# Kernel optimization log

Measured on AMD Instinct MI355X. Metric: run time of the kernel, lower is better.

The kernel has to match this reference:

```python
import jax, jax.numpy as jnp
import numpy as np

N_NODES = 100000
N_EDGES = 1600000
IN_CH = 64
HID = 64
N_CLASSES = 10
N_GRAPHS = 64


def setup_inputs() -> dict:
    key = jax.random.key(0)
    ks = jax.random.split(key, 12)
    x = jax.random.normal(ks[0], (N_NODES, IN_CH), dtype=jnp.float32)
    edge_index = jax.random.randint(ks[1], (2, N_EDGES), 0, N_NODES, dtype=jnp.int64)
    batch = jnp.sort(jax.random.randint(ks[2], (N_NODES,), 0, N_GRAPHS, dtype=jnp.int64))
    def glorot(k, shape):
        lim = 1.0 / np.sqrt(shape[1])
        return jax.random.uniform(k, shape, dtype=jnp.float32, minval=-lim, maxval=lim)
    # GraphConv layer 1: lin_rel (with bias) and lin_root (no bias)
    W1_rel = glorot(ks[3], (HID, IN_CH))
    W1_root = glorot(ks[4], (HID, IN_CH))
    b1 = glorot(ks[5], (1, IN_CH))[0, :HID] * 0 + glorot(ks[5], (HID, 1))[:, 0]
    # GraphConv layer 2
    W2_rel = glorot(ks[6], (HID, HID))
    W2_root = glorot(ks[7], (HID, HID))
    b2 = glorot(ks[8], (HID, 1))[:, 0]
    # final classifier Linear
    W_lin = glorot(ks[9], (N_CLASSES, HID))
    b_lin = glorot(ks[10], (N_CLASSES, 1))[:, 0]
    return {
        "x": x, "edge_index": edge_index, "batch": batch,
        "W1_rel": W1_rel, "W1_root": W1_root, "b1": b1,
        "W2_rel": W2_rel, "W2_root": W2_root, "b2": b2,
        "W_lin": W_lin, "b_lin": b_lin,
    }


def _graph_conv(x, src, dst, W_rel, W_root, b):
    # PyG GraphConv: out_i = W_rel @ (sum_{j->i} x_j) + b + W_root @ x_i
    agg = jax.ops.segment_sum(x[src], dst, num_segments=N_NODES)  # [N, C]
    return agg @ W_rel.T + x @ W_root.T + b


def reference(x, edge_index, batch, W1_rel, W1_root, b1, W2_rel, W2_root, b2, W_lin, b_lin):
    src, dst = edge_index[0], edge_index[1]
    h = jax.nn.relu(_graph_conv(x, src, dst, W1_rel, W1_root, b1))
    h = jax.nn.relu(_graph_conv(h, src, dst, W2_rel, W2_root, b2))
    # global mean pool over graph ids
    sums = jax.ops.segment_sum(h, batch, num_segments=N_GRAPHS)          # [G, H]
    counts = jax.ops.segment_sum(jnp.ones((h.shape[0],), h.dtype), batch, num_segments=N_GRAPHS)
    pooled = sums / jnp.maximum(counts, 1.0)[:, None]
    return pooled @ W_lin.T + b_lin  # [G, num_classes]
```

## Files before the change

### kernel.cpp

```cpp
#include <hip/hip_runtime.h>

typedef unsigned short u16;
typedef __attribute__((ext_vector_type(8))) short bf16x8;
typedef __attribute__((ext_vector_type(4))) float f32x4;

constexpr int CH = 64;
constexpr int NG = 64;
constexpr int NC = 10;
constexpr int SHIFT = 9;
constexpr int BW = 1 << SHIFT;
constexpr int EPW = 8192;

__device__ __forceinline__ void f4add(float4& a, const float4 v) {
    a.x += v.x; a.y += v.y; a.z += v.z; a.w += v.w;
}
__device__ __forceinline__ u16 f2bf(float f) {
    unsigned u = __float_as_uint(f);
    u = (u + 0x7FFFu + ((u >> 16) & 1u)) >> 16;
    return (u16)u;
}
__device__ __forceinline__ void bfacc(float4& a, unsigned lo, unsigned hi) {
    a.x += __uint_as_float(lo << 16);
    a.y += __uint_as_float(lo & 0xFFFF0000u);
    a.z += __uint_as_float(hi << 16);
    a.w += __uint_as_float(hi & 0xFFFF0000u);
}

__global__ __launch_bounds__(256) void k_bucket(const int* __restrict__ src,
                                                const int* __restrict__ dst,
                                                int* __restrict__ bcnt,
                                                int* __restrict__ bbuf,
                                                int nb, int cap, int n_edges)
{
    __shared__ int hist[256];
    __shared__ int cur[256];
    int t = threadIdx.x;
    int e0 = blockIdx.x * EPW;
    int e1 = min(e0 + EPW, n_edges);
    if (t < nb) hist[t] = 0;
    __syncthreads();
    for (int e = e0 + t; e < e1; e += 256)
        atomicAdd(&hist[dst[e] >> SHIFT], 1);
    __syncthreads();
    if (t < nb) cur[t] = atomicAdd(&bcnt[t], hist[t]);
    __syncthreads();
    for (int e = e0 + t; e < e1; e += 256) {
        int d = dst[e];
        int b = d >> SHIFT;
        int pos = atomicAdd(&cur[b], 1);
        if (pos < cap)
            bbuf[(size_t)b * cap + pos] = src[e] | ((d & (BW - 1)) << 17);
    }
}

__global__ __launch_bounds__(256) void k_bscan(const int* __restrict__ bcnt,
                                               int* __restrict__ bbase,
                                               int* __restrict__ rowptr,
                                               int nb, int n, int cap)
{
    __shared__ int lds[256];
    int t = threadIdx.x;
    int v = (t < nb) ? min(bcnt[t], cap) : 0;
    lds[t] = v;
    __syncthreads();
    for (int off = 1; off < 256; off <<= 1) {
        int u = (t >= off) ? lds[t - off] : 0;
        __syncthreads();
        lds[t] += u;
        __syncthreads();
    }
    if (t < nb) bbase[t] = lds[t] - v;
    if (t == nb - 1) { bbase[nb] = lds[t]; rowptr[n] = lds[t]; }
}

__global__ __launch_bounds__(256) void k_build(const int* __restrict__ bbuf,
                                               const int* __restrict__ bcnt,
                                               const int* __restrict__ bbase,
                                               int* __restrict__ rowptr,
                                               int* __restrict__ csr,
                                               int cap, int n)
{
    __shared__ int hist[BW];
    __shared__ int cur[BW];
    __shared__ int psum[256];
    int b = blockIdx.x;
    int t = threadIdx.x;
    int cnt = min(bcnt[b], cap);
    int base = bbase[b];
    const int* mybuf = bbuf + (size_t)b * cap;
    hist[t] = 0; hist[t + 256] = 0;
    __syncthreads();
    for (int i = t; i < cnt; i += 256)
        atomicAdd(&hist[mybuf[i] >> 17], 1);
    __syncthreads();
    int h0 = hist[2 * t], h1 = hist[2 * t + 1];
    int ps = h0 + h1;
    psum[t] = ps;
    __syncthreads();
    for (int off = 1; off < 256; off <<= 1) {
        int u = (t >= off) ? psum[t - off] : 0;
        __syncthreads();
        psum[t] += u;
        __syncthreads();
    }
    int e0 = psum[t] - ps;
    int nodeBase = b * BW;
    cur[2 * t]     = base + e0;
    cur[2 * t + 1] = base + e0 + h0;
    if (nodeBase + 2 * t < n)     rowptr[nodeBase + 2 * t]     = base + e0;
    if (nodeBase + 2 * t + 1 < n) rowptr[nodeBase + 2 * t + 1] = base + e0 + h0;
    __syncthreads();
    for (int i = t; i < cnt; i += 256) {
        int v = mybuf[i];
        int pos = atomicAdd(&cur[v >> 17], 1);
        csr[pos] = v & 0x1FFFF;
    }
}

template<bool BF16IN>
__global__ __launch_bounds__(256) void k_xform_mfma(const void* in_,
                                                    const float* __restrict__ Wrel,
                                                    const float* __restrict__ Wroot,
                                                    const float* __restrict__ bias,
                                                    u16* __restrict__ Y,
                                                    u16* R, int n, int ngroups)
{
    int lane = threadIdx.x & 63;
    int lr = lane & 15;
    int g  = lane >> 4;

    bf16x8 wf[2][4][2];
    const float* Wm[2] = { Wrel, Wroot };
#pragma unroll
    for (int m = 0; m < 2; ++m)
#pragma unroll
        for (int t = 0; t < 4; ++t)
#pragma unroll
            for (int kt = 0; kt < 2; ++kt) {
                const float* p = Wm[m] + (16 * t + lr) * CH + 32 * kt + 8 * g;
                bf16x8 v;
#pragma unroll
                for (int j = 0; j < 8; ++j) v[j] = (short)f2bf(p[j]);
                wf[m][t][kt] = v;
            }
    float bvt[4];
#pragma unroll
    for (int t = 0; t < 4; ++t) bvt[t] = bias[16 * t + lr];

    int wid = blockIdx.x * 4 + (threadIdx.x >> 6);
#pragma unroll
    for (int gi = 0; gi < 2; ++gi) {
        int grp = wid * 2 + gi;
        if (grp >= ngroups) return;
        int gbase = grp * 16;
        int arow = gbase + lr;
        if (arow >= n) arow = n - 1;

        bf16x8 af[2];
#pragma unroll
        for (int kt = 0; kt < 2; ++kt) {
            if (BF16IN) {
                const u16* hp = (const u16*)in_ + (size_t)arow * CH + kt * 32 + 8 * g;
                af[kt] = *(const bf16x8*)hp;
            } else {
                const float* xp = (const float*)in_ + (size_t)arow * CH + kt * 32 + 8 * g;
                bf16x8 v;
#pragma unroll
                for (int j = 0; j < 8; ++j) v[j] = (short)f2bf(xp[j]);
                af[kt] = v;
            }
        }

        f32x4 z = { 0.f, 0.f, 0.f, 0.f };
        f32x4 aY[4] = { z, z, z, z };
        f32x4 aR[4] = { z, z, z, z };
#pragma unroll
        for (int kt = 0; kt < 2; ++kt)
#pragma unroll
            for (int t = 0; t < 4; ++t) {
                aY[t] = __builtin_amdgcn_mfma_f32_16x16x32_bf16(af[kt], wf[0][t][kt], aY[t], 0, 0, 0);
                aR[t] = __builtin_amdgcn_mfma_f32_16x16x32_bf16(af[kt], wf[1][t][kt], aR[t], 0, 0, 0);
            }

#pragma unroll
        for (int t = 0; t < 4; ++t)
#pragma unroll
            for (int r = 0; r < 4; ++r) {
                int node = gbase + 4 * g + r;
                if (node < n) {
                    Y[(size_t)node * CH + 16 * t + lr] = f2bf(aY[t][r]);
                    R[(size_t)node * CH + 16 * t + lr] = f2bf(aR[t][r] + bvt[t]);
                }
            }
    }
}

__global__ __launch_bounds__(256) void k_gather_relu(const u16* __restrict__ Y,
                                                     const int* __restrict__ rowptr,
                                                     const int* __restrict__ csr,
                                                     u16* __restrict__ RO, int n)
{
    int lane = threadIdx.x & 63;
    int grp = lane >> 4, sub = lane & 15;
    int wid = blockIdx.x * 4 + (threadIdx.x >> 6);
    int nw = gridDim.x * 4;
    for (int node = wid; node < n; node += nw) {
        int e0 = rowptr[node], e1 = rowptr[node + 1];
        float4 a0 = make_float4(0, 0, 0, 0), a1 = a0, a2 = a0, a3 = a0;
        int e = e0;
        for (; e + 16 <= e1; e += 16) {
            int s0 = csr[e + grp],      s1 = csr[e + 4 + grp];
            int s2 = csr[e + 8 + grp],  s3 = csr[e + 12 + grp];
            uint2 p0 = *(const uint2*)(Y + (size_t)s0 * CH + sub * 4);
            uint2 p1 = *(const uint2*)(Y + (size_t)s1 * CH + sub * 4);
            uint2 p2 = *(const uint2*)(Y + (size_t)s2 * CH + sub * 4);
            uint2 p3 = *(const uint2*)(Y + (size_t)s3 * CH + sub * 4);
            bfacc(a0, p0.x, p0.y); bfacc(a1, p1.x, p1.y);
            bfacc(a2, p2.x, p2.y); bfacc(a3, p3.x, p3.y);
        }
        for (; e + 4 <= e1; e += 4) {
            int s = csr[e + grp];
            uint2 p = *(const uint2*)(Y + (size_t)s * CH + sub * 4);
            bfacc(a0, p.x, p.y);
        }
        if (e + grp < e1) {
            int s = csr[e + grp];
            uint2 p = *(const uint2*)(Y + (size_t)s * CH + sub * 4);
            bfacc(a1, p.x, p.y);
        }
        f4add(a0, a1); f4add(a2, a3); f4add(a0, a2);
        a0.x += __shfl_xor(a0.x, 16); a0.y += __shfl_xor(a0.y, 16);
        a0.z += __shfl_xor(a0.z, 16); a0.w += __shfl_xor(a0.w, 16);
        a0.x += __shfl_xor(a0.x, 32); a0.y += __shfl_xor(a0.y, 32);
        a0.z += __shfl_xor(a0.z, 32); a0.w += __shfl_xor(a0.w, 32);
        if (grp == 0) {
            uint2 pr = *(const uint2*)(RO + (size_t)node * CH + sub * 4);
            float4 r = make_float4(0, 0, 0, 0);
            bfacc(r, pr.x, pr.y);
            float4 h;
            h.x = fmaxf(a0.x + r.x, 0.f); h.y = fmaxf(a0.y + r.y, 0.f);
            h.z = fmaxf(a0.z + r.z, 0.f); h.w = fmaxf(a0.w + r.w, 0.f);
            uint2 o;
            o.x = (unsigned)f2bf(h.x) | ((unsigned)f2bf(h.y) << 16);
            o.y = (unsigned)f2bf(h.z) | ((unsigned)f2bf(h.w) << 16);
            *(uint2*)(RO + (size_t)node * CH + sub * 4) = o;
        }
    }
}

__global__ __launch_bounds__(256) void k_gather_pool(const u16* __restrict__ Y,
                                                     const u16* __restrict__ R,
                                                     const int* __restrict__ rowptr,
                                                     const int* __restrict__ csr,
                                                     const int* __restrict__ batch,
                                                     float* __restrict__ sums,
                                                     int n, int chunk)
{
    int lane = threadIdx.x & 63;
    int grp = lane >> 4, sub = lane & 15;
    int wid = blockIdx.x * 4 + (threadIdx.x >> 6);
    int nb = wid * chunk, ne = min(nb + chunk, n);
    float4 run = make_float4(0, 0, 0, 0);
    int gcur = -1;
    for (int node = nb; node < ne; ++node) {
        int e0 = rowptr[node], e1 = rowptr[node + 1];
        float4 a0 = make_float4(0, 0, 0, 0), a1 = a0, a2 = a0, a3 = a0;
        int e = e0;
        for (; e + 16 <= e1; e += 16) {
            int s0 = csr[e + grp],      s1 = csr[e + 4 + grp];
            int s2 = csr[e + 8 + grp],  s3 = csr[e + 12 + grp];
            uint2 p0 = *(const uint2*)(Y + (size_t)s0 * CH + sub * 4);
            uint2 p1 = *(const uint2*)(Y + (size_t)s1 * CH + sub * 4);
            uint2 p2 = *(const uint2*)(Y + (size_t)s2 * CH + sub * 4);
            uint2 p3 = *(const uint2*)(Y + (size_t)s3 * CH + sub * 4);
            bfacc(a0, p0.x, p0.y); bfacc(a1, p1.x, p1.y);
            bfacc(a2, p2.x, p2.y); bfacc(a3, p3.x, p3.y);
        }
        for (; e + 4 <= e1; e += 4) {
            int s = csr[e + grp];
            uint2 p = *(const uint2*)(Y + (size_t)s * CH + sub * 4);
            bfacc(a0, p.x, p.y);
        }
        if (e + grp < e1) {
            int s = csr[e + grp];
            uint2 p = *(const uint2*)(Y + (size_t)s * CH + sub * 4);
            bfacc(a1, p.x, p.y);
        }
        f4add(a0, a1); f4add(a2, a3); f4add(a0, a2);
        a0.x += __shfl_xor(a0.x, 16); a0.y += __shfl_xor(a0.y, 16);
        a0.z += __shfl_xor(a0.z, 16); a0.w += __shfl_xor(a0.w, 16);
        a0.x += __shfl_xor(a0.x, 32); a0.y += __shfl_xor(a0.y, 32);
        a0.z += __shfl_xor(a0.z, 32); a0.w += __shfl_xor(a0.w, 32);
        if (grp == 0) {
            uint2 pr = *(const uint2*)(R + (size_t)node * CH + sub * 4);
            float4 r = make_float4(0, 0, 0, 0);
            bfacc(r, pr.x, pr.y);
            float4 h;
            h.x = fmaxf(a0.x + r.x, 0.f); h.y = fmaxf(a0.y + r.y, 0.f);
            h.z = fmaxf(a0.z + r.z, 0.f); h.w = fmaxf(a0.w + r.w, 0.f);
            int g = batch[node];
            if (g != gcur) {
                if (gcur >= 0) {
                    atomicAdd(&sums[gcur * CH + sub * 4 + 0], run.x);
                    atomicAdd(&sums[gcur * CH + sub * 4 + 1], run.y);
                    atomicAdd(&sums[gcur * CH + sub * 4 + 2], run.z);
                    atomicAdd(&sums[gcur * CH + sub * 4 + 3], run.w);
                }
                run = make_float4(0, 0, 0, 0);
                gcur = g;
            }
            f4add(run, h);
        }
    }
    if (grp == 0 && gcur >= 0) {
        atomicAdd(&sums[gcur * CH + sub * 4 + 0], run.x);
        atomicAdd(&sums[gcur * CH + sub * 4 + 1], run.y);
        atomicAdd(&sums[gcur * CH + sub * 4 + 2], run.z);
        atomicAdd(&sums[gcur * CH + sub * 4 + 3], run.w);
    }
}

__global__ void k_final(const float* __restrict__ sums,
                        const int* __restrict__ batch,
                        const float* __restrict__ Wlin,
                        const float* __restrict__ blin,
                        float* __restrict__ out, int n_nodes)
{
    int t = threadIdx.x;
    if (t >= NG * NC) return;
    int g = t / NC, c = t % NC;
    int lo = 0, hi = n_nodes;
    while (lo < hi) { int mid = (lo + hi) >> 1; if (batch[mid] < g) lo = mid + 1; else hi = mid; }
    int lb = lo;
    lo = 0; hi = n_nodes;
    while (lo < hi) { int mid = (lo + hi) >> 1; if (batch[mid] < g + 1) lo = mid + 1; else hi = mid; }
    int cnt = lo - lb;
    float inv = 1.0f / fmaxf((float)cnt, 1.0f);
    float acc = blin[c];
    for (int k = 0; k < CH; ++k)
        acc += sums[g * CH + k] * inv * Wlin[c * CH + k];
    out[g * NC + c] = acc;
}

extern "C" void kernel_launch(void* const* d_in, const int* in_sizes, int n_in,
                              void* d_out, int out_size, void* d_ws, size_t ws_size,
                              hipStream_t stream)
{
    const float* x      = (const float*)d_in[0];
    const int*   ei     = (const int*)d_in[1];
    const int*   batch  = (const int*)d_in[2];
    const float* W1rel  = (const float*)d_in[3];
    const float* W1root = (const float*)d_in[4];
    const float* b1     = (const float*)d_in[5];
    const float* W2rel  = (const float*)d_in[6];
    const float* W2root = (const float*)d_in[7];
    const float* b2     = (const float*)d_in[8];
    const float* Wlin   = (const float*)d_in[9];
    const float* blin   = (const float*)d_in[10];
    float* out = (float*)d_out;

    int n_nodes = in_sizes[0] / CH;
    int n_edges = in_sizes[1] / 2;
    const int* src = ei;
    const int* dst = ei + n_edges;

    int nb  = (n_nodes + BW - 1) >> SHIFT;
    int cap = n_edges / nb + 2048;

    u16*   Ybf    = (u16*)d_ws;
    u16*   Rbf    = Ybf + (size_t)n_nodes * CH;
    int*   rowptr = (int*)(Rbf + (size_t)n_nodes * CH);
    int*   csr    = rowptr + (n_nodes + 1);
    int*   bbuf   = csr + n_edges;
    int*   bcnt   = bbuf + (size_t)nb * cap;
    int*   bbase  = bcnt + 256;
    float* sums   = (float*)(bbase + 257);

    hipMemsetAsync(bcnt, 0, 256 * sizeof(int), stream);
    int b1blocks = (n_edges + EPW - 1) / EPW;
    k_bucket<<<b1blocks, 256, 0, stream>>>(src, dst, bcnt, bbuf, nb, cap, n_edges);
    k_bscan<<<1, 256, 0, stream>>>(bcnt, bbase, rowptr, nb, n_nodes, cap);
    k_build<<<nb, 256, 0, stream>>>(bbuf, bcnt, bbase, rowptr, csr, cap, n_nodes);

    int ngroups = (n_nodes + 15) / 16;
    int xblocks = (ngroups + 7) / 8;

    k_xform_mfma<false><<<xblocks, 256, 0, stream>>>(x, W1rel, W1root, b1,
                                                     Ybf, Rbf, n_nodes, ngroups);
    k_gather_relu<<<2048, 256, 0, stream>>>(Ybf, rowptr, csr, Rbf, n_nodes);

    k_xform_mfma<true><<<xblocks, 256, 0, stream>>>(Rbf, W2rel, W2root, b2,
                                                    Ybf, Rbf, n_nodes, ngroups);
    hipMemsetAsync(sums, 0, NG * CH * sizeof(float), stream);
    int waves = 2048 * 4;
    int chunk = (n_nodes + waves - 1) / waves;
    k_gather_pool<<<2048, 256, 0, stream>>>(Ybf, Rbf, rowptr, csr, batch, sums, n_nodes, chunk);

    k_final<<<1, NG * NC, 0, stream>>>(sums, batch, Wlin, blin, out, n_nodes);
}
```

Before: 237.3 us.

## Assign each 16-lane group its own node chunk in gather kernels

The gather kernels now have each 16-lane quarter-wave own a contiguous 4-node chunk and walk its edges serially, replacing the old scheme where all four groups split one node's edges and then reduced with cross-lane shuffles. This drops the shuffle reduction and the idle lanes during the epilogue, and it reuses rowptr between consecutive nodes. The two gather kernels are merged into one template with a POOL flag. The cost is more divergence between groups with different degrees, and a launch grid sized to the node count rather than a fixed 2048 blocks.

```diff
diff --git a/kernel.cpp b/kernel.cpp
--- a/kernel.cpp
+++ b/kernel.cpp
@@ -195,116 +195,64 @@
     }
 }
 
-__global__ __launch_bounds__(256) void k_gather_relu(const u16* __restrict__ Y,
-                                                     const int* __restrict__ rowptr,
-                                                     const int* __restrict__ csr,
-                                                     u16* __restrict__ RO, int n)
+template<bool POOL>
+__global__ __launch_bounds__(256) void k_gather2(const u16* __restrict__ Y,
+                                                 const int* __restrict__ rowptr,
+                                                 const int* __restrict__ csr,
+                                                 u16* RO,
+                                                 const int* __restrict__ batch,
+                                                 float* __restrict__ sums,
+                                                 int n, int chunk)
 {
     int lane = threadIdx.x & 63;
-    int grp = lane >> 4, sub = lane & 15;
-    int wid = blockIdx.x * 4 + (threadIdx.x >> 6);
-    int nw = gridDim.x * 4;
-    for (int node = wid; node < n; node += nw) {
-        int e0 = rowptr[node], e1 = rowptr[node + 1];
-        float4 a0 = make_float4(0, 0, 0, 0), a1 = a0, a2 = a0, a3 = a0;
+    int sub = lane & 15;
+    int grp = lane >> 4;
+    int gid = (blockIdx.x * 4 + (threadIdx.x >> 6)) * 4 + grp;
+    int nb = gid * chunk;
+    if (nb >= n) return;
+    int ne = min(nb + chunk, n);
+    float4 run = make_float4(0, 0, 0, 0);
+    int gcur = -1;
+    int e0 = rowptr[nb];
+    for (int node = nb; node < ne; ++node) {
+        int e1 = rowptr[node + 1];
+        float4 accA = make_float4(0, 0, 0, 0), accB = accA;
         int e = e0;
-        for (; e + 16 <= e1; e += 16) {
-            int s0 = csr[e + grp],      s1 = csr[e + 4 + grp];
-            int s2 = csr[e + 8 + grp],  s3 = csr[e + 12 + grp];
+        for (; e + 4 <= e1; e += 4) {
+            int s0 = csr[e + 0], s1 = csr[e + 1];
+            int s2 = csr[e + 2], s3 = csr[e + 3];
             uint2 p0 = *(const uint2*)(Y + (size_t)s0 * CH + sub * 4);
             uint2 p1 = *(const uint2*)(Y + (size_t)s1 * CH + sub * 4);
             uint2 p2 = *(const uint2*)(Y + (size_t)s2 * CH + sub * 4);
             uint2 p3 = *(const uint2*)(Y + (size_t)s3 * CH + sub * 4);
-            bfacc(a0, p0.x, p0.y); bfacc(a1, p1.x, p1.y);
-            bfacc(a2, p2.x, p2.y); bfacc(a3, p3.x, p3.y);
+            bfacc(accA, p0.x, p0.y); bfacc(accB, p1.x, p1.y);
+            bfacc(accA, p2.x, p2.y); bfacc(accB, p3.x, p3.y);
         }
-        for (; e + 4 <= e1; e += 4) {
-            int s = csr[e + grp];
+        for (; e < e1; ++e) {
+            int s = csr[e];
             uint2 p = *(const uint2*)(Y + (size_t)s * CH + sub * 4);
-            bfacc(a0, p.x, p.y);
+            bfacc(accA, p.x, p.y);
         }
-        if (e + grp < e1) {
-            int s = csr[e + grp];
-            uint2 p = *(const uint2*)(Y + (size_t)s * CH + sub * 4);
-            bfacc(a1, p.x, p.y);
-        }
-        f4add(a0, a1); f4add(a2, a3); f4add(a0, a2);
-        a0.x += __shfl_xor(a0.x, 16); a0.y += __shfl_xor(a0.y, 16);
-        a0.z += __shfl_xor(a0.z, 16); a0.w += __shfl_xor(a0.w, 16);
-        a0.x += __shfl_xor(a0.x, 32); a0.y += __shfl_xor(a0.y, 32);
-        a0.z += __shfl_xor(a0.z, 32); a0.w += __shfl_xor(a0.w, 32);
-        if (grp == 0) {
-            uint2 pr = *(const uint2*)(RO + (size_t)node * CH + sub * 4);
-            float4 r = make_float4(0, 0, 0, 0);
-            bfacc(r, pr.x, pr.y);
-            float4 h;
-            h.x = fmaxf(a0.x + r.x, 0.f); h.y = fmaxf(a0.y + r.y, 0.f);
-            h.z = fmaxf(a0.z + r.z, 0.f); h.w = fmaxf(a0.w + r.w, 0.f);
+        e0 = e1;
+        uint2 pr = *(const uint2*)(RO + (size_t)node * CH + sub * 4);
+        float4 r = make_float4(0, 0, 0, 0);
+        bfacc(r, pr.x, pr.y);
+        f4add(accA, accB);
+        float4 h;
+        h.x = fmaxf(accA.x + r.x, 0.f); h.y = fmaxf(accA.y + r.y, 0.f);
+        h.z = fmaxf(accA.z + r.z, 0.f); h.w = fmaxf(accA.w + r.w, 0.f);
+        if (!POOL) {
             uint2 o;
             o.x = (unsigned)f2bf(h.x) | ((unsigned)f2bf(h.y) << 16);
             o.y = (unsigned)f2bf(h.z) | ((unsigned)f2bf(h.w) << 16);
             *(uint2*)(RO + (size_t)node * CH + sub * 4) = o;
-        }
-    }
-}
-
-__global__ __launch_bounds__(256) void k_gather_pool(const u16* __restrict__ Y,
-                                                     const u16* __restrict__ R,
-                                                     const int* __restrict__ rowptr,
-                                                     const int* __restrict__ csr,
-                                                     const int* __restrict__ batch,
-                                                     float* __restrict__ sums,
-                                                     int n, int chunk)
-{
-    int lane = threadIdx.x & 63;
-    int grp = lane >> 4, sub = lane & 15;
-    int wid = blockIdx.x * 4 + (threadIdx.x >> 6);
-    int nb = wid * chunk, ne = min(nb + chunk, n);
-    float4 run = make_float4(0, 0, 0, 0);
-    int gcur = -1;
-    for (int node = nb; node < ne; ++node) {
-        int e0 = rowptr[node], e1 = rowptr[node + 1];
-        float4 a0 = make_float4(0, 0, 0, 0), a1 = a0, a2 = a0, a3 = a0;
-        int e = e0;
-        for (; e + 16 <= e1; e += 16) {
-            int s0 = csr[e + grp],      s1 = csr[e + 4 + grp];
-            int s2 = csr[e + 8 + grp],  s3 = csr[e + 12 + grp];
-            uint2 p0 = *(const uint2*)(Y + (size_t)s0 * CH + sub * 4);
-            uint2 p1 = *(const uint2*)(Y + (size_t)s1 * CH + sub * 4);
-            uint2 p2 = *(const uint2*)(Y + (size_t)s2 * CH + sub * 4);
-            uint2 p3 = *(const uint2*)(Y + (size_t)s3 * CH + sub * 4);
-            bfacc(a0, p0.x, p0.y); bfacc(a1, p1.x, p1.y);
-            bfacc(a2, p2.x, p2.y); bfacc(a3, p3.x, p3.y);
-        }
-        for (; e + 4 <= e1; e += 4) {
-            int s = csr[e + grp];
-            uint2 p = *(const uint2*)(Y + (size_t)s * CH + sub * 4);
-            bfacc(a0, p.x, p.y);
-        }
-        if (e + grp < e1) {
-            int s = csr[e + grp];
-            uint2 p = *(const uint2*)(Y + (size_t)s * CH + sub * 4);
-            bfacc(a1, p.x, p.y);
-        }
-        f4add(a0, a1); f4add(a2, a3); f4add(a0, a2);
-        a0.x += __shfl_xor(a0.x, 16); a0.y += __shfl_xor(a0.y, 16);
-        a0.z += __shfl_xor(a0.z, 16); a0.w += __shfl_xor(a0.w, 16);
-        a0.x += __shfl_xor(a0.x, 32); a0.y += __shfl_xor(a0.y, 32);
-        a0.z += __shfl_xor(a0.z, 32); a0.w += __shfl_xor(a0.w, 32);
-        if (grp == 0) {
-            uint2 pr = *(const uint2*)(R + (size_t)node * CH + sub * 4);
-            float4 r = make_float4(0, 0, 0, 0);
-            bfacc(r, pr.x, pr.y);
-            float4 h;
-            h.x = fmaxf(a0.x + r.x, 0.f); h.y = fmaxf(a0.y + r.y, 0.f);
-            h.z = fmaxf(a0.z + r.z, 0.f); h.w = fmaxf(a0.w + r.w, 0.f);
+        } else {
             int g = batch[node];
             if (g != gcur) {
                 if (gcur >= 0) {
-                    atomicAdd(&sums[gcur * CH + sub * 4 + 0], run.x);
-                    atomicAdd(&sums[gcur * CH + sub * 4 + 1], run.y);
-                    atomicAdd(&sums[gcur * CH + sub * 4 + 2], run.z);
-                    atomicAdd(&sums[gcur * CH + sub * 4 + 3], run.w);
+                    float* s = sums + gcur * CH + sub * 4;
+                    atomicAdd(s + 0, run.x); atomicAdd(s + 1, run.y);
+                    atomicAdd(s + 2, run.z); atomicAdd(s + 3, run.w);
                 }
                 run = make_float4(0, 0, 0, 0);
                 gcur = g;
@@ -312,11 +260,10 @@
             f4add(run, h);
         }
     }
-    if (grp == 0 && gcur >= 0) {
-        atomicAdd(&sums[gcur * CH + sub * 4 + 0], run.x);
-        atomicAdd(&sums[gcur * CH + sub * 4 + 1], run.y);
-        atomicAdd(&sums[gcur * CH + sub * 4 + 2], run.z);
-        atomicAdd(&sums[gcur * CH + sub * 4 + 3], run.w);
+    if (POOL && gcur >= 0) {
+        float* s = sums + gcur * CH + sub * 4;
+        atomicAdd(s + 0, run.x); atomicAdd(s + 1, run.y);
+        atomicAdd(s + 2, run.z); atomicAdd(s + 3, run.w);
     }
 }
 
@@ -382,19 +329,23 @@
     k_bscan<<<1, 256, 0, stream>>>(bcnt, bbase, rowptr, nb, n_nodes, cap);
     k_build<<<nb, 256, 0, stream>>>(bbuf, bcnt, bbase, rowptr, csr, cap, n_nodes);
 
-    int ngroups = (n_nodes + 15) / 16;
-    int xblocks = (ngroups + 7) / 8;
+    int ngroups16 = (n_nodes + 15) / 16;
+    int xblocks = (ngroups16 + 7) / 8;
+
+    int chunk = 4;
+    int gg = (n_nodes + chunk - 1) / chunk;
+    int gblocks = (gg + 15) / 16;
 
     k_xform_mfma<false><<<xblocks, 256, 0, stream>>>(x, W1rel, W1root, b1,
-                                                     Ybf, Rbf, n_nodes, ngroups);
-    k_gather_relu<<<2048, 256, 0, stream>>>(Ybf, rowptr, csr, Rbf, n_nodes);
+                                                     Ybf, Rbf, n_nodes, ngroups16);
+    k_gather2<false><<<gblocks, 256, 0, stream>>>(Ybf, rowptr, csr, Rbf,
+                                                  batch, sums, n_nodes, chunk);
 
     k_xform_mfma<true><<<xblocks, 256, 0, stream>>>(Rbf, W2rel, W2root, b2,
-                                                    Ybf, Rbf, n_nodes, ngroups);
+                                                    Ybf, Rbf, n_nodes, ngroups16);
     hipMemsetAsync(sums, 0, NG * CH * sizeof(float), stream);
-    int waves = 2048 * 4;
-    int chunk = (n_nodes + waves - 1) / waves;
-    k_gather_pool<<<2048, 256, 0, stream>>>(Ybf, Rbf, rowptr, csr, batch, sums, n_nodes, chunk);
+    k_gather2<true><<<gblocks, 256, 0, stream>>>(Ybf, rowptr, csr, Rbf,
+                                                 batch, sums, n_nodes, chunk);
 
     k_final<<<1, NG * NC, 0, stream>>>(sums, batch, Wlin, blin, out, n_nodes);
 }
```

New measurement: 288.1 us. 21.4% more time.
